# Kernel tuning notes

Hardware: AMD Instinct MI355X
Metric: run time of the kernel (lower is better)

The kernel has to match this reference:

```python
import jax, jax.numpy as jnp
import numpy as np

EPS = 1e-5  # torch nn.LayerNorm default

def _ln(z, g, b):
    m = jnp.mean(z, axis=-1, keepdims=True)
    v = jnp.mean((z - m) ** 2, axis=-1, keepdims=True)
    return (z - m) * jax.lax.rsqrt(v + EPS) * g + b

def setup_inputs() -> dict:
    key = jax.random.key(0)
    ks = jax.random.split(key, 5)
    S, B, I, H = 2048, 1, 2048, 2048
    stdv = 1.0 / float(np.sqrt(H))
    u = lambda k, shape: jax.random.uniform(k, shape, jnp.float32, -stdv, stdv)
    return {
        "x": jax.random.normal(ks[0], (S, B, I), jnp.float32),
        "w_ih": u(ks[1], (4 * H, I)),
        "w_hh": u(ks[2], (4 * H, H)),
        "b_ih": u(ks[3], (4 * H,)),
        "b_hh": u(ks[4], (4 * H,)),
        # LN params for [input_gate, forget_gate, cell_gate, output_gate, cy]
        "ln_gamma": jnp.ones((5, H), jnp.float32),
        "ln_beta": jnp.zeros((5, H), jnp.float32),
    }

def reference(x, w_ih, w_hh, b_ih, b_hh, ln_gamma, ln_beta):
    S, B, I = x.shape
    H = w_hh.shape[1]
    # hoist the input projection out of the recurrence: one big GEMM
    xg = jnp.einsum('sbi,gi->sbg', x, w_ih) + b_ih + b_hh  # (S, B, 4H)
    h0 = jnp.zeros((B, H), x.dtype)
    c0 = jnp.zeros((B, H), x.dtype)

    def step(carry, xg_t):
        h, c = carry
        gates = xg_t + h @ w_hh.T                     # (B, 4H)
        i_, f_, g_, o_ = jnp.split(gates, 4, axis=-1)
        i = jax.nn.sigmoid(_ln(i_, ln_gamma[0], ln_beta[0]))
        f = jax.nn.sigmoid(_ln(f_, ln_gamma[1], ln_beta[1]))
        g = jnp.tanh(_ln(g_, ln_gamma[2], ln_beta[2]))
        o = jax.nn.sigmoid(_ln(o_, ln_gamma[3], ln_beta[3]))
        cy = _ln(f * c + i * g, ln_gamma[4], ln_beta[4])
        hy = o * jnp.tanh(cy)
        return (hy, cy), hy

    (hy, cy), hs = jax.lax.scan(step, (h0, c0), xg)   # hs: (S, B, H)
    # torch: y = stack([h[-1] for h in ht]).unsqueeze(1) -> last batch row, (S,1,H)
    y = hs[:, -1, :][:, None, :]
    return y, hy, cy
```

## Files before the change

### kernel.cpp

```cpp
#include <hip/hip_runtime.h>

typedef float f32x2 __attribute__((ext_vector_type(2)));
typedef float f32x4 __attribute__((ext_vector_type(4)));
typedef short bf16x8 __attribute__((ext_vector_type(8)));
typedef _Float16 f16x2 __attribute__((ext_vector_type(2)));
typedef _Float16 f16x4 __attribute__((ext_vector_type(4)));
typedef _Float16 f16x8 __attribute__((ext_vector_type(8)));

#define SEQ 2048
#define HD 2048
#define NG 8192
#define KD 2048
#define NB 256
#define NT 512
#define PAD_CH 136

__device__ __forceinline__ unsigned short f32_to_bf16_rne(float f) {
    unsigned int u = __float_as_uint(f);
    u += 0x7FFFu + ((u >> 16) & 1u);
    return (unsigned short)(u >> 16);
}

__global__ void cvt_f16_kernel(const float* __restrict__ in, _Float16* __restrict__ out, int n) {
    for (int i = blockIdx.x * blockDim.x + threadIdx.x; i < n; i += gridDim.x * blockDim.x)
        out[i] = (_Float16)in[i];
}

__global__ __launch_bounds__(256) void gemm_xg(
    const float* __restrict__ A,
    const float* __restrict__ B,
    const float* __restrict__ bih, const float* __restrict__ bhh,
    float* __restrict__ C)
{
    __shared__ unsigned short As[128 * 32];
    __shared__ unsigned short Bs[128 * 32];
    const int tid = threadIdx.x;
    const int bm = blockIdx.x, bn = blockIdx.y;
    const int wave = tid >> 6, lane = tid & 63;
    const int wr = wave >> 1, wc = wave & 1;
    const int l15 = lane & 15, l4 = lane >> 4;

    f32x4 acc[4][4];
    #pragma unroll
    for (int i = 0; i < 4; ++i)
        #pragma unroll
        for (int j = 0; j < 4; ++j) {
            f32x4 z = {0.f, 0.f, 0.f, 0.f};
            acc[i][j] = z;
        }

    for (int k0 = 0; k0 < KD; k0 += 32) {
        #pragma unroll
        for (int i = 0; i < 2; ++i) {
            int idx = tid + i * 256;
            int row = idx >> 2, c8 = idx & 3;
            const float* ga = A + (size_t)(bm * 128 + row) * KD + k0 + c8 * 8;
            float4 a0 = *(const float4*)ga;
            float4 a1 = *(const float4*)(ga + 4);
            bf16x8 av;
            av[0] = (short)f32_to_bf16_rne(a0.x); av[1] = (short)f32_to_bf16_rne(a0.y);
            av[2] = (short)f32_to_bf16_rne(a0.z); av[3] = (short)f32_to_bf16_rne(a0.w);
            av[4] = (short)f32_to_bf16_rne(a1.x); av[5] = (short)f32_to_bf16_rne(a1.y);
            av[6] = (short)f32_to_bf16_rne(a1.z); av[7] = (short)f32_to_bf16_rne(a1.w);
            *(bf16x8*)&As[row * 32 + c8 * 8] = av;
            const float* gb = B + (size_t)(bn * 128 + row) * KD + k0 + c8 * 8;
            float4 b0 = *(const float4*)gb;
            float4 b1 = *(const float4*)(gb + 4);
            bf16x8 bv;
            bv[0] = (short)f32_to_bf16_rne(b0.x); bv[1] = (short)f32_to_bf16_rne(b0.y);
            bv[2] = (short)f32_to_bf16_rne(b0.z); bv[3] = (short)f32_to_bf16_rne(b0.w);
            bv[4] = (short)f32_to_bf16_rne(b1.x); bv[5] = (short)f32_to_bf16_rne(b1.y);
            bv[6] = (short)f32_to_bf16_rne(b1.z); bv[7] = (short)f32_to_bf16_rne(b1.w);
            *(bf16x8*)&Bs[row * 32 + c8 * 8] = bv;
        }
        __syncthreads();
        bf16x8 af[4], bfr[4];
        #pragma unroll
        for (int m = 0; m < 4; ++m) af[m] = *(const bf16x8*)&As[(wr * 64 + m * 16 + l15) * 32 + l4 * 8];
        #pragma unroll
        for (int n = 0; n < 4; ++n) bfr[n] = *(const bf16x8*)&Bs[(wc * 64 + n * 16 + l15) * 32 + l4 * 8];
        #pragma unroll
        for (int m = 0; m < 4; ++m)
            #pragma unroll
            for (int n = 0; n < 4; ++n)
                acc[m][n] = __builtin_amdgcn_mfma_f32_16x16x32_bf16(af[m], bfr[n], acc[m][n], 0, 0, 0);
        __syncthreads();
    }
    #pragma unroll
    for (int m = 0; m < 4; ++m) {
        #pragma unroll
        for (int n = 0; n < 4; ++n) {
            int col = bn * 128 + wc * 64 + n * 16 + l15;
            float bias = bih[col] + bhh[col];
            int row0 = bm * 128 + wr * 64 + m * 16 + l4 * 4;
            #pragma unroll
            for (int r = 0; r < 4; ++r)
                C[(size_t)(row0 + r) * NG + col] = acc[m][n][r] + bias;
        }
    }
}

__device__ __forceinline__ void st_llc16(float* p, f32x4 v) {
    asm volatile("global_store_dwordx4 %0, %1, off sc0 sc1" :: "v"(p), "v"(v) : "memory");
}
__device__ __forceinline__ void st_llc8(float* p, f32x2 v) {
    asm volatile("global_store_dwordx2 %0, %1, off sc0 sc1" :: "v"(p), "v"(v) : "memory");
}
__device__ __forceinline__ void ld_llc_issue4(const float* p0, const float* p1,
                                              const float* p2, const float* p3,
                                              f32x4& a, f32x4& b, f32x4& c, f32x4& d) {
    asm volatile(
        "global_load_dwordx4 %0, %4, off sc0 sc1\n\t"
        "global_load_dwordx4 %1, %5, off sc0 sc1\n\t"
        "global_load_dwordx4 %2, %6, off sc0 sc1\n\t"
        "global_load_dwordx4 %3, %7, off sc0 sc1"
        : "=&v"(a), "=&v"(b), "=&v"(c), "=&v"(d)
        : "v"(p0), "v"(p1), "v"(p2), "v"(p3)
        : "memory");
}
__device__ __forceinline__ void wait_vm0_4(f32x4& a, f32x4& b, f32x4& c, f32x4& d) {
    asm volatile("s_waitcnt vmcnt(0)" : "+v"(a), "+v"(b), "+v"(c), "+v"(d) :: "memory");
    __builtin_amdgcn_sched_barrier(0);
}
__device__ __forceinline__ void ld_llc_4x4_wait(const float* p, f32x4& a, f32x4& b, f32x4& c, f32x4& d) {
    asm volatile(
        "global_load_dwordx4 %0, %4, off sc0 sc1\n\t"
        "global_load_dwordx4 %1, %4, off offset:16 sc0 sc1\n\t"
        "global_load_dwordx4 %2, %4, off offset:32 sc0 sc1\n\t"
        "global_load_dwordx4 %3, %4, off offset:48 sc0 sc1\n\t"
        "s_waitcnt vmcnt(0)"
        : "=&v"(a), "=&v"(b), "=&v"(c), "=&v"(d)
        : "v"(p)
        : "memory");
    __builtin_amdgcn_sched_barrier(0);
}
__device__ __forceinline__ void ld_gl16(const float* p, f32x4& a) {
    asm volatile("global_load_dwordx4 %0, %1, off" : "=&v"(a) : "v"(p) : "memory");
}

__device__ __forceinline__ float rcpf(float x) { return __builtin_amdgcn_rcpf(x); }
__device__ __forceinline__ float rsqf(float x) { return __builtin_amdgcn_rsqf(x); }
__device__ __forceinline__ float sigf(float x) { return rcpf(1.0f + __expf(-x)); }
__device__ __forceinline__ float tanhfast(float x) {
    float ax = fabsf(x);
    float e = __expf(-2.0f * ax);
    return __builtin_copysignf((1.0f - e) * rcpf(1.0f + e), x);
}

#define ROOT_OFF (8 * 64)
#define RELAY_OFF (9 * 64)

__global__ __launch_bounds__(512, 2) void lstm_rec(
    const float* __restrict__ xg,
    const _Float16* __restrict__ Whh,
    const float* __restrict__ gamma,
    const float* __restrict__ beta,
    float* __restrict__ gates,
    float* __restrict__ partials,
    unsigned* __restrict__ barctl,
    float* __restrict__ yout)
{
    __shared__ _Float16 hlds[16 * PAD_CH];
    __shared__ __align__(16) float red2[16];
    __shared__ __align__(16) float statsmem[8];

    const int b = blockIdx.x;
    const int t = threadIdx.x;
    const int wave = t >> 6, lane = t & 63;
    const int p = t * 4;

    unsigned* grpcnt = barctl + (b >> 5) * 64;
    unsigned* rootcnt = barctl + ROOT_OFF;
    unsigned* relay = barctl + RELAY_OFF + (b >> 5) * 64;

    const int row = t >> 4, sub = t & 15;
    const int grow = b * 32 + row;

    f16x8 wreg[16];
    {
        const _Float16* wsrc = Whh + (size_t)grow * HD + sub * 128;
        #pragma unroll
        for (int i = 0; i < 16; ++i) wreg[i] = *(const f16x8*)(wsrc + i * 8);
    }
    for (int k = t; k < 16 * PAD_CH; k += NT) hlds[k] = (_Float16)0.0f;

    float4 gm[4], bt[4];
    #pragma unroll
    for (int g = 0; g < 4; ++g) {
        gm[g] = *(const float4*)&gamma[g * HD + p];
        bt[g] = *(const float4*)&beta[g * HD + p];
    }
    float4 gm4 = *(const float4*)&gamma[4 * HD + p];
    float4 bt4 = *(const float4*)&beta[4 * HD + p];

    float* hyout = yout + (size_t)SEQ * HD;
    float* cyout = hyout + HD;
    const float invH = 1.0f / 2048.0f;

    float cprev[4] = {0.f, 0.f, 0.f, 0.f};

    f32x4 xg4 = {0.f, 0.f, 0.f, 0.f};
    if (lane == 0) xg4 = *(const f32x4*)(xg + b * 32 + wave * 4);

    const _Float16* hch = hlds + sub * PAD_CH;
    __syncthreads();

    for (int step = 0; step < SEQ; ++step) {
        float* gb = gates + (size_t)(step & 1) * NG;
        float* pb = partials + (size_t)(step & 1) * (NB * 8 * 2);
        const unsigned gen = (unsigned)(step + 1);

        float accv[4] = {0.f, 0.f, 0.f, 0.f};
        #pragma unroll
        for (int i = 0; i < 16; ++i) {
            f16x8 hv = *(const f16x8*)(hch + i * 8);
            const f16x2* w2 = (const f16x2*)&wreg[i];
            const f16x2* h2 = (const f16x2*)&hv;
            float x = accv[i & 3];
            x = __builtin_amdgcn_fdot2(w2[0], h2[0], x, false);
            x = __builtin_amdgcn_fdot2(w2[1], h2[1], x, false);
            x = __builtin_amdgcn_fdot2(w2[2], h2[2], x, false);
            x = __builtin_amdgcn_fdot2(w2[3], h2[3], x, false);
            accv[i & 3] = x;
        }
        float r = (accv[0] + accv[1]) + (accv[2] + accv[3]);
        #pragma unroll
        for (int off = 1; off < 16; off <<= 1) r += __shfl_xor(r, off);
        float r1 = __shfl(r, 16), r2 = __shfl(r, 32), r3 = __shfl(r, 48);
        if (lane == 0) {
            f32x4 gv4 = {r + xg4[0], r1 + xg4[1], r2 + xg4[2], r3 + xg4[3]};
            st_llc16(&gb[b * 32 + wave * 4], gv4);
            float s4 = (gv4[0] + gv4[1]) + (gv4[2] + gv4[3]);
            float q4 = (gv4[0] * gv4[0] + gv4[1] * gv4[1]) + (gv4[2] * gv4[2] + gv4[3] * gv4[3]);
            f32x2 pq = {s4, q4};
            st_llc8(&pb[(b * 8 + wave) * 2], pq);
        }

        __syncthreads();

        if (t == 0) {
            asm volatile("" ::: "memory");
            unsigned o1 = __hip_atomic_fetch_add(grpcnt, 1u, __ATOMIC_RELAXED, __HIP_MEMORY_SCOPE_AGENT);
            if (o1 == gen * 32u - 1u) {
                unsigned o2 = __hip_atomic_fetch_add(rootcnt, 1u, __ATOMIC_RELAXED, __HIP_MEMORY_SCOPE_AGENT);
                if (o2 == gen * 8u - 1u) {
                    #pragma unroll
                    for (int g = 0; g < 8; ++g)
                        __hip_atomic_store(barctl + RELAY_OFF + g * 64, gen,
                                           __ATOMIC_RELAXED, __HIP_MEMORY_SCOPE_AGENT);
                }
            }
        }
        for (;;) {
            unsigned rv = __hip_atomic_load(relay, __ATOMIC_RELAXED, __HIP_MEMORY_SCOPE_AGENT);
            if (rv >= gen) break;
            __builtin_amdgcn_s_sleep(1);
        }
        asm volatile("" ::: "memory");

        f32x4 gq[4];
        ld_llc_issue4(&gb[0 * HD + p], &gb[1 * HD + p], &gb[2 * HD + p], &gb[3 * HD + p],
                      gq[0], gq[1], gq[2], gq[3]);
        if (lane == 0 && step + 1 < SEQ)
            ld_gl16(xg + (size_t)(step + 1) * NG + b * 32 + wave * 4, xg4);

        if (wave < 4) {
            f32x4 pa, pbv, pc, pd;
            ld_llc_4x4_wait(&pb[wave * 1024 + lane * 16], pa, pbv, pc, pd);
            float s = ((pa[0] + pa[2]) + (pbv[0] + pbv[2])) + ((pc[0] + pc[2]) + (pd[0] + pd[2]));
            float q = ((pa[1] + pa[3]) + (pbv[1] + pbv[3])) + ((pc[1] + pc[3]) + (pd[1] + pd[3]));
            #pragma unroll
            for (int off = 1; off < 64; off <<= 1) { s += __shfl_xor(s, off); q += __shfl_xor(q, off); }
            if (lane == 0) {
                float m = s * invH;
                statsmem[wave * 2] = m;
                statsmem[wave * 2 + 1] = rsqf(q * invH - m * m + 1e-5f);
            }
        }
        __syncthreads();

        wait_vm0_4(gq[0], gq[1], gq[2], gq[3]);
        float mg[4], rg[4];
        {
            const f32x4* sm = (const f32x4*)statsmem;
            f32x4 s0 = sm[0], s1 = sm[1];
            mg[0] = s0[0]; rg[0] = s0[1]; mg[1] = s0[2]; rg[1] = s0[3];
            mg[2] = s1[0]; rg[2] = s1[1]; mg[3] = s1[2]; rg[3] = s1[3];
        }

        float rcv[4], og4[4];
        float s2 = 0.f, q2 = 0.f;
        #pragma unroll
        for (int j = 0; j < 4; ++j) {
            float li = (gq[0][j] - mg[0]) * rg[0] * ((const float*)&gm[0])[j] + ((const float*)&bt[0])[j];
            float lf = (gq[1][j] - mg[1]) * rg[1] * ((const float*)&gm[1])[j] + ((const float*)&bt[1])[j];
            float lg = (gq[2][j] - mg[2]) * rg[2] * ((const float*)&gm[2])[j] + ((const float*)&bt[2])[j];
            float lo = (gq[3][j] - mg[3]) * rg[3] * ((const float*)&gm[3])[j] + ((const float*)&bt[3])[j];
            float ig = sigf(li);
            float fg = sigf(lf);
            float gg = tanhfast(lg);
            float og = sigf(lo);
            float rv = fg * cprev[j] + ig * gg;
            rcv[j] = rv; og4[j] = og;
            s2 += rv; q2 += rv * rv;
        }
        #pragma unroll
        for (int off = 1; off < 64; off <<= 1) { s2 += __shfl_xor(s2, off); q2 += __shfl_xor(q2, off); }
        if (lane == 0) { red2[wave] = s2; red2[8 + wave] = q2; }
        __syncthreads();

        float mc, rc;
        {
            const f32x4* r4 = (const f32x4*)red2;
            f32x4 sa = r4[0], sb = r4[1], qa = r4[2], qb = r4[3];
            float s = ((sa[0] + sa[1]) + (sa[2] + sa[3])) + ((sb[0] + sb[1]) + (sb[2] + sb[3]));
            float q = ((qa[0] + qa[1]) + (qa[2] + qa[3])) + ((qb[0] + qb[1]) + (qb[2] + qb[3]));
            mc = s * invH;
            rc = rsqf(q * invH - mc * mc + 1e-5f);
        }

        float hvf[4], lcf[4];
        f16x4 hh;
        #pragma unroll
        for (int j = 0; j < 4; ++j) {
            float lc = (rcv[j] - mc) * rc * ((const float*)&gm4)[j] + ((const float*)&bt4)[j];
            cprev[j] = lc;
            float th = tanhfast(lc);
            float hv = og4[j] * th;
            hvf[j] = hv; lcf[j] = lc;
            hh[j] = (_Float16)hv;
        }
        *(f16x4*)&hlds[(t >> 5) * PAD_CH + (p & 127)] = hh;

        if ((t >> 1) == b) {
            float4 ho = {hvf[0], hvf[1], hvf[2], hvf[3]};
            *(float4*)&yout[(size_t)step * HD + p] = ho;
            if (step == SEQ - 1) {
                *(float4*)&hyout[p] = ho;
                float4 co = {lcf[0], lcf[1], lcf[2], lcf[3]};
                *(float4*)&cyout[p] = co;
            }
        }
        __syncthreads();
    }
}

extern "C" void kernel_launch(void* const* d_in, const int* in_sizes, int n_in,
                              void* d_out, int out_size, void* d_ws, size_t ws_size,
                              hipStream_t stream) {
    const float* x   = (const float*)d_in[0];
    const float* wih = (const float*)d_in[1];
    const float* whh = (const float*)d_in[2];
    const float* bih = (const float*)d_in[3];
    const float* bhh = (const float*)d_in[4];
    const float* gam = (const float*)d_in[5];
    const float* bet = (const float*)d_in[6];
    float* out = (float*)d_out;

    char* ws = (char*)d_ws;
    size_t off = 0;
    auto carve = [&](size_t bytes) -> void* {
        void* pp = ws + off;
        off += (bytes + 255) & ~(size_t)255;
        return pp;
    };
    float* xg      = (float*)carve(sizeof(float) * (size_t)SEQ * NG);
    _Float16* whhf = (_Float16*)carve(sizeof(_Float16) * (size_t)NG * HD);
    float* gates   = (float*)carve(sizeof(float) * 2 * NG);
    float* parts   = (float*)carve(sizeof(float) * 2 * NB * 8 * 2);
    unsigned* barctl = (unsigned*)carve(sizeof(unsigned) * 17 * 64);

    cvt_f16_kernel<<<2048, 256, 0, stream>>>(whh, whhf, NG * HD);
    dim3 ggrid(16, 64);
    gemm_xg<<<ggrid, 256, 0, stream>>>(x, wih, bih, bhh, xg);
    hipMemsetAsync(barctl, 0, sizeof(unsigned) * 17 * 64, stream);

    void* args[] = { (void*)&xg, (void*)&whhf, (void*)&gam, (void*)&bet,
                     (void*)&gates, (void*)&parts, (void*)&barctl, (void*)&out };
    hipLaunchCooperativeKernel((void*)lstm_rec, dim3(NB), dim3(NT), args, 0, stream);
}
```

Measured before the change: 10.07 ms.

## Flatten grid barrier to per-group done flags and overlap partial-stat loads

Replaces the two-level grid barrier (group counter, then root counter, then relay broadcast) with per-group done flags that every wave polls together: lanes 0-7 each read one group flag and the wave exits when all are set. This removes one serialized atomic hop from the per-step critical path. The partial-statistics loads are now issued before the gate loads, and waits use counted vmcnt so the stats arrive first. Plain __syncthreads are replaced by s_barrier preceded only by an lgkmcnt wait. In exchange, all 256 blocks now poll 8 flags instead of one, which adds L2 traffic, and the hand-counted vmcnt values must match the actual number of outstanding loads.

```diff
diff --git a/kernel.cpp b/kernel.cpp
--- a/kernel.cpp
+++ b/kernel.cpp
@@ -106,6 +106,16 @@
 __device__ __forceinline__ void st_llc8(float* p, f32x2 v) {
     asm volatile("global_store_dwordx2 %0, %1, off sc0 sc1" :: "v"(p), "v"(v) : "memory");
 }
+__device__ __forceinline__ void ld_llc_issue_p(const float* p, f32x4& a, f32x4& b, f32x4& c, f32x4& d) {
+    asm volatile(
+        "global_load_dwordx4 %0, %4, off sc0 sc1\n\t"
+        "global_load_dwordx4 %1, %4, off offset:16 sc0 sc1\n\t"
+        "global_load_dwordx4 %2, %4, off offset:32 sc0 sc1\n\t"
+        "global_load_dwordx4 %3, %4, off offset:48 sc0 sc1"
+        : "=&v"(a), "=&v"(b), "=&v"(c), "=&v"(d)
+        : "v"(p)
+        : "memory");
+}
 __device__ __forceinline__ void ld_llc_issue4(const float* p0, const float* p1,
                                               const float* p2, const float* p3,
                                               f32x4& a, f32x4& b, f32x4& c, f32x4& d) {
@@ -118,24 +128,20 @@
         : "v"(p0), "v"(p1), "v"(p2), "v"(p3)
         : "memory");
 }
-__device__ __forceinline__ void wait_vm0_4(f32x4& a, f32x4& b, f32x4& c, f32x4& d) {
-    asm volatile("s_waitcnt vmcnt(0)" : "+v"(a), "+v"(b), "+v"(c), "+v"(d) :: "memory");
-    __builtin_amdgcn_sched_barrier(0);
-}
-__device__ __forceinline__ void ld_llc_4x4_wait(const float* p, f32x4& a, f32x4& b, f32x4& c, f32x4& d) {
-    asm volatile(
-        "global_load_dwordx4 %0, %4, off sc0 sc1\n\t"
-        "global_load_dwordx4 %1, %4, off offset:16 sc0 sc1\n\t"
-        "global_load_dwordx4 %2, %4, off offset:32 sc0 sc1\n\t"
-        "global_load_dwordx4 %3, %4, off offset:48 sc0 sc1\n\t"
-        "s_waitcnt vmcnt(0)"
-        : "=&v"(a), "=&v"(b), "=&v"(c), "=&v"(d)
-        : "v"(p)
-        : "memory");
-    __builtin_amdgcn_sched_barrier(0);
-}
 __device__ __forceinline__ void ld_gl16(const float* p, f32x4& a) {
     asm volatile("global_load_dwordx4 %0, %1, off" : "=&v"(a) : "v"(p) : "memory");
+}
+__device__ __forceinline__ void wait_vm5(f32x4& a, f32x4& b, f32x4& c, f32x4& d) {
+    asm volatile("s_waitcnt vmcnt(5)" : "+v"(a), "+v"(b), "+v"(c), "+v"(d) :: "memory");
+    __builtin_amdgcn_sched_barrier(0);
+}
+__device__ __forceinline__ void wait_vm1(f32x4& a, f32x4& b, f32x4& c, f32x4& d) {
+    asm volatile("s_waitcnt vmcnt(1)" : "+v"(a), "+v"(b), "+v"(c), "+v"(d) :: "memory");
+    __builtin_amdgcn_sched_barrier(0);
+}
+__device__ __forceinline__ void wait_vm0_1(f32x4& a) {
+    asm volatile("s_waitcnt vmcnt(0)" : "+v"(a) :: "memory");
+    __builtin_amdgcn_sched_barrier(0);
 }
 
 __device__ __forceinline__ float rcpf(float x) { return __builtin_amdgcn_rcpf(x); }
@@ -147,8 +153,16 @@
     return __builtin_copysignf((1.0f - e) * rcpf(1.0f + e), x);
 }
 
-#define ROOT_OFF (8 * 64)
-#define RELAY_OFF (9 * 64)
+__device__ __forceinline__ void bar_lgkm() {
+    asm volatile("s_waitcnt lgkmcnt(0)" ::: "memory");
+    __builtin_amdgcn_s_barrier();
+}
+__device__ __forceinline__ void bar_full() {
+    asm volatile("s_waitcnt vmcnt(0) lgkmcnt(0)" ::: "memory");
+    __builtin_amdgcn_s_barrier();
+}
+
+#define DONE_OFF (8 * 64)
 
 __global__ __launch_bounds__(512, 2) void lstm_rec(
     const float* __restrict__ xg,
@@ -170,8 +184,6 @@
     const int p = t * 4;
 
     unsigned* grpcnt = barctl + (b >> 5) * 64;
-    unsigned* rootcnt = barctl + ROOT_OFF;
-    unsigned* relay = barctl + RELAY_OFF + (b >> 5) * 64;
 
     const int row = t >> 4, sub = t & 15;
     const int grow = b * 32 + row;
@@ -227,37 +239,37 @@
         #pragma unroll
         for (int off = 1; off < 16; off <<= 1) r += __shfl_xor(r, off);
         float r1 = __shfl(r, 16), r2 = __shfl(r, 32), r3 = __shfl(r, 48);
+        wait_vm0_1(xg4);
         if (lane == 0) {
-            f32x4 gv4 = {r + xg4[0], r1 + xg4[1], r2 + xg4[2], r3 + xg4[3]};
+            float g0 = r + xg4[0], g1 = r1 + xg4[1], g2 = r2 + xg4[2], g3 = r3 + xg4[3];
+            f32x4 gv4 = {g0, g1, g2, g3};
             st_llc16(&gb[b * 32 + wave * 4], gv4);
-            float s4 = (gv4[0] + gv4[1]) + (gv4[2] + gv4[3]);
-            float q4 = (gv4[0] * gv4[0] + gv4[1] * gv4[1]) + (gv4[2] * gv4[2] + gv4[3] * gv4[3]);
-            f32x2 pq = {s4, q4};
+            f32x2 pq = {(g0 + g1) + (g2 + g3),
+                        (g0 * g0 + g1 * g1) + (g2 * g2 + g3 * g3)};
             st_llc8(&pb[(b * 8 + wave) * 2], pq);
         }
 
-        __syncthreads();
+        bar_full();
 
         if (t == 0) {
             asm volatile("" ::: "memory");
             unsigned o1 = __hip_atomic_fetch_add(grpcnt, 1u, __ATOMIC_RELAXED, __HIP_MEMORY_SCOPE_AGENT);
-            if (o1 == gen * 32u - 1u) {
-                unsigned o2 = __hip_atomic_fetch_add(rootcnt, 1u, __ATOMIC_RELAXED, __HIP_MEMORY_SCOPE_AGENT);
-                if (o2 == gen * 8u - 1u) {
-                    #pragma unroll
-                    for (int g = 0; g < 8; ++g)
-                        __hip_atomic_store(barctl + RELAY_OFF + g * 64, gen,
-                                           __ATOMIC_RELAXED, __HIP_MEMORY_SCOPE_AGENT);
-                }
-            }
+            if (o1 == gen * 32u - 1u)
+                __hip_atomic_store(barctl + DONE_OFF + (b >> 5) * 64, gen,
+                                   __ATOMIC_RELAXED, __HIP_MEMORY_SCOPE_AGENT);
         }
         for (;;) {
-            unsigned rv = __hip_atomic_load(relay, __ATOMIC_RELAXED, __HIP_MEMORY_SCOPE_AGENT);
-            if (rv >= gen) break;
+            unsigned v = 0xFFFFFFFFu;
+            if (lane < 8)
+                v = __hip_atomic_load(barctl + DONE_OFF + lane * 64, __ATOMIC_RELAXED, __HIP_MEMORY_SCOPE_AGENT);
+            if (__all(v >= gen)) break;
             __builtin_amdgcn_s_sleep(1);
         }
         asm volatile("" ::: "memory");
 
+        f32x4 pa, pbv, pc, pd;
+        if (wave < 4)
+            ld_llc_issue_p(&pb[wave * 1024 + lane * 16], pa, pbv, pc, pd);
         f32x4 gq[4];
         ld_llc_issue4(&gb[0 * HD + p], &gb[1 * HD + p], &gb[2 * HD + p], &gb[3 * HD + p],
                       gq[0], gq[1], gq[2], gq[3]);
@@ -265,8 +277,7 @@
             ld_gl16(xg + (size_t)(step + 1) * NG + b * 32 + wave * 4, xg4);
 
         if (wave < 4) {
-            f32x4 pa, pbv, pc, pd;
-            ld_llc_4x4_wait(&pb[wave * 1024 + lane * 16], pa, pbv, pc, pd);
+            wait_vm5(pa, pbv, pc, pd);
             float s = ((pa[0] + pa[2]) + (pbv[0] + pbv[2])) + ((pc[0] + pc[2]) + (pd[0] + pd[2]));
             float q = ((pa[1] + pa[3]) + (pbv[1] + pbv[3])) + ((pc[1] + pc[3]) + (pd[1] + pd[3]));
             #pragma unroll
@@ -277,9 +288,9 @@
                 statsmem[wave * 2 + 1] = rsqf(q * invH - m * m + 1e-5f);
             }
         }
-        __syncthreads();
-
-        wait_vm0_4(gq[0], gq[1], gq[2], gq[3]);
+        bar_lgkm();
+
+        wait_vm1(gq[0], gq[1], gq[2], gq[3]);
         float mg[4], rg[4];
         {
             const f32x4* sm = (const f32x4*)statsmem;
@@ -307,7 +318,7 @@
         #pragma unroll
         for (int off = 1; off < 64; off <<= 1) { s2 += __shfl_xor(s2, off); q2 += __shfl_xor(q2, off); }
         if (lane == 0) { red2[wave] = s2; red2[8 + wave] = q2; }
-        __syncthreads();
+        bar_lgkm();
 
         float mc, rc;
         {
@@ -341,7 +352,7 @@
                 *(float4*)&cyout[p] = co;
             }
         }
-        __syncthreads();
+        bar_lgkm();
     }
 }
 
@@ -368,12 +379,12 @@
     _Float16* whhf = (_Float16*)carve(sizeof(_Float16) * (size_t)NG * HD);
     float* gates   = (float*)carve(sizeof(float) * 2 * NG);
     float* parts   = (float*)carve(sizeof(float) * 2 * NB * 8 * 2);
-    unsigned* barctl = (unsigned*)carve(sizeof(unsigned) * 17 * 64);
+    unsigned* barctl = (unsigned*)carve(sizeof(unsigned) * 16 * 64);
 
     cvt_f16_kernel<<<2048, 256, 0, stream>>>(whh, whhf, NG * HD);
     dim3 ggrid(16, 64);
     gemm_xg<<<ggrid, 256, 0, stream>>>(x, wih, bih, bhh, xg);
-    hipMemsetAsync(barctl, 0, sizeof(unsigned) * 17 * 64, stream);
+    hipMemsetAsync(barctl, 0, sizeof(unsigned) * 16 * 64, stream);
 
     void* args[] = { (void*)&xg, (void*)&whhf, (void*)&gam, (void*)&bet,
                      (void*)&gates, (void*)&parts, (void*)&barctl, (void*)&out };
```

New measurement: 9.958 ms. About the same (-1.1%).
